# Kernel tuning notes

Hardware: AMD Instinct MI355X
Metric: run time of the kernel (lower is better)

Reference implementation:

```python
import jax, jax.numpy as jnp
import numpy as np

N, M, C, CSKIP, K = 16384, 4096, 256, 128, 3
BIG = 1e10  # distance penalty for cross-batch pairs


def setup_inputs() -> dict:
    key = jax.random.key(0)
    ks = jax.random.split(key, 6)
    return {
        "x": jax.random.normal(ks[0], (M, C), jnp.float32),
        "pos": jax.random.normal(ks[1], (M, 3), jnp.float32),
        "batch": jnp.zeros((M,), jnp.int32),
        "x_skip": jax.random.normal(ks[2], (N, CSKIP), jnp.float32),
        "pos_skip": jax.random.normal(ks[3], (N, 3), jnp.float32),
        "batch_skip": jnp.zeros((N,), jnp.int32),
        "W1": jax.random.normal(ks[4], (C + CSKIP, 256), jnp.float32) * (1.0 / np.sqrt(C + CSKIP)),
        "b1": jnp.zeros((256,), jnp.float32),
        "W2": jax.random.normal(ks[5], (256, 256), jnp.float32) * (1.0 / np.sqrt(256)),
        "b2": jnp.zeros((256,), jnp.float32),
    }


def _knn_idx(pos, pos_skip, batch, batch_skip, k):
    # Squared distances via GEMM form: [N, M]
    a2 = jnp.sum(pos_skip * pos_skip, axis=-1, keepdims=True)      # [N,1]
    b2 = jnp.sum(pos * pos, axis=-1)[None, :]                       # [1,M]
    d2 = a2 + b2 - 2.0 * (pos_skip @ pos.T)                         # [N,M]
    d2 = jnp.where(batch_skip[:, None] != batch[None, :], BIG, d2)
    _, idx = jax.lax.top_k(-d2, k)                                  # [N,k]
    return idx


def reference(x, pos, batch, x_skip, pos_skip, batch_skip, W1, b1, W2, b2):
    idx = _knn_idx(pos, pos_skip, batch, batch_skip, K)             # [N,k] coarse neighbor ids
    # Exact squared dist recomputed from gathered positions (matches torch diff path)
    diff = pos_skip[:, None, :] - pos[idx]                          # [N,k,3]
    d2 = jnp.sum(diff * diff, axis=-1, keepdims=True)               # [N,k,1]
    w = 1.0 / (d2 + 1e-8)                                           # inverse-distance weights
    wsum = jnp.sum(w, axis=1, keepdims=True)                        # per-row scatter_add == sum over k
    w = w / (wsum + 1e-8)
    x_interp = jnp.sum(w * x[idx], axis=1)                          # [N,C]
    h = jnp.concatenate([x_interp, x_skip], axis=1)                 # [N,C+C']
    h = jax.nn.relu(h @ W1 + b1)
    h = jax.nn.relu(h @ W2 + b2)
    return h
```

## Files before the change

### kernel.cpp

```cpp
#include <hip/hip_runtime.h>

typedef float     f4   __attribute__((ext_vector_type(4)));
typedef float     f32x4 __attribute__((ext_vector_type(4)));
typedef _Float16  h8   __attribute__((ext_vector_type(8)));
typedef _Float16  h4   __attribute__((ext_vector_type(4)));
typedef int       i4   __attribute__((ext_vector_type(4)));

#define NQ   16384
#define MP   4096
#define CF   256
#define CSK  128
#define K1   384
#define HID  256
#define QB   16

__global__ __launch_bounds__(256) void knn_kernel(
    const float* __restrict__ pos,
    const float* __restrict__ pos_skip,
    int*   __restrict__ idx_out,
    float* __restrict__ w_out)
{
    __shared__ float          px[MP];
    __shared__ float          py[MP];
    __shared__ float          pz[MP];
    __shared__ unsigned short ci[QB][96];
    __shared__ unsigned short ci2[QB][16][3];

    const int tid = threadIdx.x;

    for (int j = tid; j < MP; j += 256) {
        px[j] = pos[3*j+0];
        py[j] = pos[3*j+1];
        pz[j] = pos[3*j+2];
    }
    __syncthreads();

    const int lane = tid & 63;
    const int wv   = tid >> 6;

    float qx[4], qy[4], qz[4];
    #pragma unroll
    for (int k = 0; k < 4; k++) {
        const int q = blockIdx.x * QB + wv * 4 + k;
        qx[k] = pos_skip[3*q+0];
        qy[k] = pos_skip[3*q+1];
        qz[k] = pos_skip[3*q+2];
    }

    unsigned K0[4], K1v[4], K2[4];
    #pragma unroll
    for (int k = 0; k < 4; k++) { K0[k] = ~0u; K1v[k] = ~0u; K2[k] = ~0u; }

    #define EVAL(PX, PY, PZ, J)                                               \
        _Pragma("unroll")                                                     \
        for (int k = 0; k < 4; k++) {                                         \
            const float dx = qx[k] - (PX), dy = qy[k] - (PY),                 \
                        dz = qz[k] - (PZ);                                    \
            const float dd = fmaf(dx, dx, fmaf(dy, dy, dz * dz));             \
            const unsigned key = (__float_as_uint(dd) & 0xFFFFF000u) | (J);   \
            const unsigned h0 = max(K0[k], key);                              \
            K0[k] = min(K0[k], key);                                          \
            const unsigned n1 = min(K1v[k], h0);                              \
            const unsigned h1 = max(K1v[k], h0);                              \
            K1v[k] = n1;                                                      \
            K2[k] = min(K2[k], h1);                                           \
        }

    float c0x = px[lane],       c1x = px[lane + 64],
          c2x = px[lane + 128], c3x = px[lane + 192];
    float c0y = py[lane],       c1y = py[lane + 64],
          c2y = py[lane + 128], c3y = py[lane + 192];
    float c0z = pz[lane],       c1z = pz[lane + 64],
          c2z = pz[lane + 128], c3z = pz[lane + 192];

    for (int it = 0; it < 64; it += 4) {
        const unsigned jb = it * 64 + lane;
        const float nx0 = px[jb + 256], nx1 = px[jb + 320],
                    nx2 = px[jb + 384], nx3 = px[jb + 448];
        const float ny0 = py[jb + 256], ny1 = py[jb + 320],
                    ny2 = py[jb + 384], ny3 = py[jb + 448];
        const float nz0 = pz[jb + 256], nz1 = pz[jb + 320],
                    nz2 = pz[jb + 384], nz3 = pz[jb + 448];
        EVAL(c0x, c0y, c0z, jb);
        EVAL(c1x, c1y, c1z, jb + 64);
        EVAL(c2x, c2y, c2z, jb + 128);
        EVAL(c3x, c3y, c3z, jb + 192);
        c0x = nx0; c1x = nx1; c2x = nx2; c3x = nx3;
        c0y = ny0; c1y = ny1; c2y = ny2; c3y = ny3;
        c0z = nz0; c1z = nz1; c2z = nz2; c3z = nz3;
    }
    #undef EVAL

    #pragma unroll
    for (int k = 0; k < 4; k++) {
        const unsigned b0 = (unsigned)__builtin_amdgcn_ds_swizzle((int)K0[k],  0x041F);
        const unsigned b1 = (unsigned)__builtin_amdgcn_ds_swizzle((int)K1v[k], 0x041F);
        const unsigned b2 = (unsigned)__builtin_amdgcn_ds_swizzle((int)K2[k],  0x041F);
        const unsigned m0 = min(K0[k], b0);
        const unsigned c1 = max(K0[k], b0);
        const unsigned d0 = min(K1v[k], b1), d1 = max(K1v[k], b1);
        const unsigned m1 = min(c1, d0);
        const unsigned m2 = min(min(max(c1, d0), d1), min(K2[k], b2));
        if (!(lane & 1)) {
            const int q = wv * 4 + k;
            const int pr = lane >> 1;
            ci[q][pr*3+0] = (unsigned short)(m0 & 0xFFFu);
            ci[q][pr*3+1] = (unsigned short)(m1 & 0xFFFu);
            ci[q][pr*3+2] = (unsigned short)(m2 & 0xFFFu);
        }
    }
    __syncthreads();

    {
        const int q    = tid >> 4;
        const int part = tid & 15;
        const int g    = blockIdx.x * QB + q;
        const double qxd = (double)pos_skip[3*g+0];
        const double qyd = (double)pos_skip[3*g+1];
        const double qzd = (double)pos_skip[3*g+2];
        const double a2d = qxd*qxd + qyd*qyd + qzd*qzd;

        double e0 = 1e300, e1 = 1e300, e2 = 1e300;
        int    j0 = 0,     j1 = 0,     j2 = 0;
        #pragma unroll
        for (int c = 0; c < 6; c++) {
            const int j = ci[q][part*6 + c];
            const double pxd = (double)px[j], pyd = (double)py[j],
                         pzd = (double)pz[j];
            const double b2  = pxd*pxd + pyd*pyd + pzd*pzd;
            const double dot = qxd*pxd + qyd*pyd + qzd*pzd;
            const double d   = (a2d + b2) - 2.0 * dot;
            if (d < e2) {
                if (d < e1) {
                    e2 = e1; j2 = j1;
                    if (d < e0) { e1 = e0; j1 = j0; e0 = d; j0 = j; }
                    else        { e1 = d;  j1 = j; }
                } else { e2 = d; j2 = j; }
            }
        }
        ci2[q][part][0] = (unsigned short)j0;
        ci2[q][part][1] = (unsigned short)j1;
        ci2[q][part][2] = (unsigned short)j2;
    }
    __syncthreads();

    if (tid < QB) {
        const int g = blockIdx.x * QB + tid;
        const double qxd = (double)pos_skip[3*g+0];
        const double qyd = (double)pos_skip[3*g+1];
        const double qzd = (double)pos_skip[3*g+2];
        const double a2d = qxd*qxd + qyd*qyd + qzd*qzd;

        double e0 = 1e300, e1 = 1e300, e2 = 1e300;
        int    j0 = 0,     j1 = 0,     j2 = 0;
        for (int p = 0; p < 16; p++) {
            #pragma unroll
            for (int s = 0; s < 3; s++) {
                const int j = ci2[tid][p][s];
                const double pxd = (double)px[j], pyd = (double)py[j],
                             pzd = (double)pz[j];
                const double b2  = pxd*pxd + pyd*pyd + pzd*pzd;
                const double dot = qxd*pxd + qyd*pyd + qzd*pzd;
                const double d   = (a2d + b2) - 2.0 * dot;
                if (d < e2) {
                    if (d < e1) {
                        e2 = e1; j2 = j1;
                        if (d < e0) { e1 = e0; j1 = j0; e0 = d; j0 = j; }
                        else        { e1 = d;  j1 = j; }
                    } else { e2 = d; j2 = j; }
                }
            }
        }
        const float sx = pos_skip[3*g+0], sy = pos_skip[3*g+1], sz = pos_skip[3*g+2];
        const int jj[3] = { j0, j1, j2 };
        float wv3[3];
        #pragma unroll
        for (int k = 0; k < 3; k++) {
            const float dx = sx - px[jj[k]], dy = sy - py[jj[k]],
                        dz = sz - pz[jj[k]];
            const float dd = dx*dx + dy*dy + dz*dz;
            wv3[k] = 1.0f / (dd + 1e-8f);
        }
        const float inv = 1.0f / (wv3[0] + wv3[1] + wv3[2] + 1e-8f);
        #pragma unroll
        for (int k = 0; k < 3; k++) {
            idx_out[g*3+k] = jj[k];
            w_out[g*3+k]   = wv3[k] * inv;
        }
    }
}

__global__ __launch_bounds__(256) void wconv_kernel(
    const float* __restrict__ W1, const float* __restrict__ W2,
    _Float16* __restrict__ Wt1, _Float16* __restrict__ Wt2)
{
    const int i = blockIdx.x * 256 + threadIdx.x;
    if (i < K1 * HID) {
        const int k = i >> 8, n = i & 255;
        Wt1[(size_t)(k >> 5) * 8192 + ((k >> 3) & 3) * 2048 + n * 8 + (k & 7)]
            = (_Float16)W1[i];
    } else {
        const int i2 = i - K1 * HID;
        const int k = i2 >> 8, n = i2 & 255;
        Wt2[(size_t)(k >> 5) * 8192 + ((k >> 3) & 3) * 2048 + n * 8 + (k & 7)]
            = (_Float16)W2[i2];
    }
}

__global__ __launch_bounds__(256) void mlp_kernel(
    const float* __restrict__ x,
    const float* __restrict__ x_skip,
    const _Float16* __restrict__ Wt1,
    const _Float16* __restrict__ Wt2,
    const float* __restrict__ b1,
    const float* __restrict__ b2,
    const int*   __restrict__ nidx,
    const float* __restrict__ nw,
    float* __restrict__ out)
{
    __shared__ _Float16 As[32][392];
    _Float16 (*Hs)[264] = reinterpret_cast<_Float16 (*)[264]>(&As[0][0]);

    const int tid  = threadIdx.x;
    const int row0 = blockIdx.x * 32;

    {
        const int r   = tid >> 3;
        const int sub = tid & 7;
        const int g   = row0 + r;
        const int j0 = nidx[g*3+0], j1 = nidx[g*3+1], j2 = nidx[g*3+2];
        const float w0 = nw[g*3+0], w1 = nw[g*3+1], w2 = nw[g*3+2];
        const f4* xa = (const f4*)(x + (size_t)j0 * CF);
        const f4* xb = (const f4*)(x + (size_t)j1 * CF);
        const f4* xc = (const f4*)(x + (size_t)j2 * CF);
        const f4* xs = (const f4*)(x_skip + (size_t)g * CSK);
        #pragma unroll
        for (int t = 0; t < 8; t++) {
            const int c4 = t * 8 + sub;
            const f4 a = xa[c4], b = xb[c4], c = xc[c4];
            const f4 v = a * w0 + b * w1 + c * w2;
            h4 hv; hv[0]=(_Float16)v[0]; hv[1]=(_Float16)v[1];
                   hv[2]=(_Float16)v[2]; hv[3]=(_Float16)v[3];
            *(h4*)&As[r][c4 * 4] = hv;
        }
        #pragma unroll
        for (int t = 0; t < 4; t++) {
            const int c4 = t * 8 + sub;
            const f4 v = xs[c4];
            h4 hv; hv[0]=(_Float16)v[0]; hv[1]=(_Float16)v[1];
                   hv[2]=(_Float16)v[2]; hv[3]=(_Float16)v[3];
            *(h4*)&As[r][CF + c4 * 4] = hv;
        }
    }

    const int ln   = tid & 15;
    const int quad = (tid >> 4) & 3;
    const int wv_  = tid >> 6;
    const int nb   = wv_ * 64;
    const int q8   = quad * 8;

    const _Float16* w1b = Wt1 + quad * 2048 + (size_t)(nb + ln) * 8;
    const _Float16* w2b = Wt2 + quad * 2048 + (size_t)(nb + ln) * 8;

    f32x4 acc[2][4];
    #pragma unroll
    for (int mt = 0; mt < 2; mt++)
        #pragma unroll
        for (int nt = 0; nt < 4; nt++) acc[mt][nt] = (f32x4)0.0f;

    h8 B[3][4];
    #pragma unroll
    for (int s = 0; s < 3; s++)
        #pragma unroll
        for (int nt = 0; nt < 4; nt++)
            B[s][nt] = *(const h8*)(w1b + (size_t)s * 8192 + nt * 128);

    __syncthreads();

    #pragma unroll
    for (int kb = 0; kb < 12; kb++) {
        const int s = kb % 3;
        h8 ha[2];
        #pragma unroll
        for (int mt = 0; mt < 2; mt++)
            ha[mt] = *(const h8*)&As[mt*16 + ln][kb*32 + q8];
        h8 hb[4];
        #pragma unroll
        for (int nt = 0; nt < 4; nt++) hb[nt] = B[s][nt];
        if (kb < 9) {
            #pragma unroll
            for (int nt = 0; nt < 4; nt++)
                B[s][nt] = *(const h8*)(w1b + (size_t)(kb+3) * 8192 + nt * 128);
        } else {
            #pragma unroll
            for (int nt = 0; nt < 4; nt++)
                B[s][nt] = *(const h8*)(w2b + (size_t)(kb-9) * 8192 + nt * 128);
        }
        #pragma unroll
        for (int mt = 0; mt < 2; mt++)
            #pragma unroll
            for (int nt = 0; nt < 4; nt++)
                acc[mt][nt] = __builtin_amdgcn_mfma_f32_16x16x32_f16(
                    ha[mt], hb[nt], acc[mt][nt], 0, 0, 0);
    }
    __syncthreads();

    #pragma unroll
    for (int nt = 0; nt < 4; nt++) {
        const int n = nb + nt*16 + ln;
        const float bv = b1[n];
        #pragma unroll
        for (int mt = 0; mt < 2; mt++) {
            #pragma unroll
            for (int r = 0; r < 4; r++) {
                const int m = mt*16 + quad*4 + r;
                Hs[m][n] = (_Float16)fmaxf(acc[mt][nt][r] + bv, 0.0f);
            }
            acc[mt][nt] = (f32x4)0.0f;
        }
    }
    __syncthreads();

    #pragma unroll
    for (int kb = 0; kb < 8; kb++) {
        const int s = kb % 3;
        h8 ha[2];
        #pragma unroll
        for (int mt = 0; mt < 2; mt++)
            ha[mt] = *(const h8*)&Hs[mt*16 + ln][kb*32 + q8];
        h8 hb[4];
        #pragma unroll
        for (int nt = 0; nt < 4; nt++) hb[nt] = B[s][nt];
        if (kb < 5) {
            #pragma unroll
            for (int nt = 0; nt < 4; nt++)
                B[s][nt] = *(const h8*)(w2b + (size_t)(kb+3) * 8192 + nt * 128);
        }
        #pragma unroll
        for (int mt = 0; mt < 2; mt++)
            #pragma unroll
            for (int nt = 0; nt < 4; nt++)
                acc[mt][nt] = __builtin_amdgcn_mfma_f32_16x16x32_f16(
                    ha[mt], hb[nt], acc[mt][nt], 0, 0, 0);
    }

    #pragma unroll
    for (int nt = 0; nt < 4; nt++) {
        const int n = nb + nt*16 + ln;
        const float bv = b2[n];
        #pragma unroll
        for (int mt = 0; mt < 2; mt++)
            #pragma unroll
            for (int r = 0; r < 4; r++) {
                const int m = mt*16 + quad*4 + r;
                out[(size_t)(row0 + m) * HID + n] = fmaxf(acc[mt][nt][r] + bv, 0.0f);
            }
    }
}

extern "C" void kernel_launch(void* const* d_in, const int* in_sizes, int n_in,
                              void* d_out, int out_size, void* d_ws, size_t ws_size,
                              hipStream_t stream) {
    const float* x         = (const float*)d_in[0];
    const float* pos       = (const float*)d_in[1];
    const float* x_skip    = (const float*)d_in[3];
    const float* pos_skip  = (const float*)d_in[4];
    const float* W1        = (const float*)d_in[6];
    const float* b1        = (const float*)d_in[7];
    const float* W2        = (const float*)d_in[8];
    const float* b2        = (const float*)d_in[9];
    float* out = (float*)d_out;

    char* ws = (char*)d_ws;
    int*      nidx = (int*)ws;
    float*    nw   = (float*)(ws + 196608);
    _Float16* Wt1  = (_Float16*)(ws + 393216);
    _Float16* Wt2  = (_Float16*)(ws + 589824);

    wconv_kernel<<<(K1*HID + HID*HID) / 256, 256, 0, stream>>>(W1, W2, Wt1, Wt2);
    knn_kernel<<<NQ / QB, 256, 0, stream>>>(pos, pos_skip, nidx, nw);
    mlp_kernel<<<NQ / 32, 256, 0, stream>>>(x, x_skip, Wt1, Wt2, b1, b2, nidx, nw, out);
}
```

Baseline: 129.7 us.

## Fuse weight conversion into kNN, store positions as fp16, widen MLP blocks

The standalone weight-conversion launch is removed and its work spread across the first 1024 kNN blocks, 160 elements each. kNN candidate positions are now held in shared memory as fp16 (xy packed plus z), which halves LDS footprint and traffic, while the fp64 refinement stages read positions straight from global memory. The MLP kernel now processes 64 rows per block with 512 threads, so each weight fragment load is shared by more rows. The fp16 coarse distances may lose accuracy in candidate selection, and the refinement stages now pay global-memory gathers instead of LDS reads.

```diff
diff --git a/kernel.cpp b/kernel.cpp
--- a/kernel.cpp
+++ b/kernel.cpp
@@ -4,6 +4,7 @@
 typedef float     f32x4 __attribute__((ext_vector_type(4)));
 typedef _Float16  h8   __attribute__((ext_vector_type(8)));
 typedef _Float16  h4   __attribute__((ext_vector_type(4)));
+typedef _Float16  h2   __attribute__((ext_vector_type(2)));
 typedef int       i4   __attribute__((ext_vector_type(4)));
 
 #define NQ   16384
@@ -17,21 +18,40 @@
 __global__ __launch_bounds__(256) void knn_kernel(
     const float* __restrict__ pos,
     const float* __restrict__ pos_skip,
+    const float* __restrict__ W1,
+    const float* __restrict__ W2,
+    _Float16* __restrict__ Wt1,
+    _Float16* __restrict__ Wt2,
     int*   __restrict__ idx_out,
     float* __restrict__ w_out)
 {
-    __shared__ float          px[MP];
-    __shared__ float          py[MP];
-    __shared__ float          pz[MP];
+    __shared__ h2             hxy[MP];
+    __shared__ _Float16       hz[MP];
     __shared__ unsigned short ci[QB][96];
     __shared__ unsigned short ci2[QB][16][3];
 
     const int tid = threadIdx.x;
 
+    {
+        const int i = blockIdx.x * 160 + tid;
+        if (tid < 160) {
+            if (i < K1 * HID) {
+                const int k = i >> 8, n = i & 255;
+                Wt1[(size_t)(k >> 5) * 8192 + ((k >> 3) & 3) * 2048 + n * 8 + (k & 7)]
+                    = (_Float16)W1[i];
+            } else {
+                const int i2 = i - K1 * HID;
+                const int k = i2 >> 8, n = i2 & 255;
+                Wt2[(size_t)(k >> 5) * 8192 + ((k >> 3) & 3) * 2048 + n * 8 + (k & 7)]
+                    = (_Float16)W2[i2];
+            }
+        }
+    }
+
     for (int j = tid; j < MP; j += 256) {
-        px[j] = pos[3*j+0];
-        py[j] = pos[3*j+1];
-        pz[j] = pos[3*j+2];
+        h2 v; v[0] = (_Float16)pos[3*j+0]; v[1] = (_Float16)pos[3*j+1];
+        hxy[j] = v;
+        hz[j]  = (_Float16)pos[3*j+2];
     }
     __syncthreads();
 
@@ -51,45 +71,44 @@
     #pragma unroll
     for (int k = 0; k < 4; k++) { K0[k] = ~0u; K1v[k] = ~0u; K2[k] = ~0u; }
 
-    #define EVAL(PX, PY, PZ, J)                                               \
-        _Pragma("unroll")                                                     \
-        for (int k = 0; k < 4; k++) {                                         \
-            const float dx = qx[k] - (PX), dy = qy[k] - (PY),                 \
-                        dz = qz[k] - (PZ);                                    \
-            const float dd = fmaf(dx, dx, fmaf(dy, dy, dz * dz));             \
-            const unsigned key = (__float_as_uint(dd) & 0xFFFFF000u) | (J);   \
-            const unsigned h0 = max(K0[k], key);                              \
-            K0[k] = min(K0[k], key);                                          \
-            const unsigned n1 = min(K1v[k], h0);                              \
-            const unsigned h1 = max(K1v[k], h0);                              \
-            K1v[k] = n1;                                                      \
-            K2[k] = min(K2[k], h1);                                           \
-        }
-
-    float c0x = px[lane],       c1x = px[lane + 64],
-          c2x = px[lane + 128], c3x = px[lane + 192];
-    float c0y = py[lane],       c1y = py[lane + 64],
-          c2y = py[lane + 128], c3y = py[lane + 192];
-    float c0z = pz[lane],       c1z = pz[lane + 64],
-          c2z = pz[lane + 128], c3z = pz[lane + 192];
+    #define EVALP(XY, Z, J)                                                   \
+        {                                                                     \
+            const float fx = (float)(XY)[0], fy = (float)(XY)[1],             \
+                        fz = (float)(Z);                                      \
+            _Pragma("unroll")                                                 \
+            for (int k = 0; k < 4; k++) {                                     \
+                const float dx = qx[k] - fx, dy = qy[k] - fy,                 \
+                            dz = qz[k] - fz;                                  \
+                const float dd = fmaf(dx, dx, fmaf(dy, dy, dz * dz));         \
+                const unsigned key = (__float_as_uint(dd) & 0xFFFFF000u) | (J);\
+                const unsigned h0 = max(K0[k], key);                          \
+                K0[k] = min(K0[k], key);                                      \
+                const unsigned n1 = min(K1v[k], h0);                          \
+                const unsigned h1 = max(K1v[k], h0);                          \
+                K1v[k] = n1;                                                  \
+                K2[k] = min(K2[k], h1);                                       \
+            }                                                                 \
+        }
+
+    h2 cxy0 = hxy[lane],       cxy1 = hxy[lane + 64],
+       cxy2 = hxy[lane + 128], cxy3 = hxy[lane + 192];
+    _Float16 cz0 = hz[lane],       cz1 = hz[lane + 64],
+             cz2 = hz[lane + 128], cz3 = hz[lane + 192];
 
     for (int it = 0; it < 64; it += 4) {
         const unsigned jb = it * 64 + lane;
-        const float nx0 = px[jb + 256], nx1 = px[jb + 320],
-                    nx2 = px[jb + 384], nx3 = px[jb + 448];
-        const float ny0 = py[jb + 256], ny1 = py[jb + 320],
-                    ny2 = py[jb + 384], ny3 = py[jb + 448];
-        const float nz0 = pz[jb + 256], nz1 = pz[jb + 320],
-                    nz2 = pz[jb + 384], nz3 = pz[jb + 448];
-        EVAL(c0x, c0y, c0z, jb);
-        EVAL(c1x, c1y, c1z, jb + 64);
-        EVAL(c2x, c2y, c2z, jb + 128);
-        EVAL(c3x, c3y, c3z, jb + 192);
-        c0x = nx0; c1x = nx1; c2x = nx2; c3x = nx3;
-        c0y = ny0; c1y = ny1; c2y = ny2; c3y = ny3;
-        c0z = nz0; c1z = nz1; c2z = nz2; c3z = nz3;
-    }
-    #undef EVAL
+        const h2 nxy0 = hxy[jb + 256], nxy1 = hxy[jb + 320],
+                 nxy2 = hxy[jb + 384], nxy3 = hxy[jb + 448];
+        const _Float16 nz0 = hz[jb + 256], nz1 = hz[jb + 320],
+                       nz2 = hz[jb + 384], nz3 = hz[jb + 448];
+        EVALP(cxy0, cz0, jb);
+        EVALP(cxy1, cz1, jb + 64);
+        EVALP(cxy2, cz2, jb + 128);
+        EVALP(cxy3, cz3, jb + 192);
+        cxy0 = nxy0; cxy1 = nxy1; cxy2 = nxy2; cxy3 = nxy3;
+        cz0 = nz0; cz1 = nz1; cz2 = nz2; cz3 = nz3;
+    }
+    #undef EVALP
 
     #pragma unroll
     for (int k = 0; k < 4; k++) {
@@ -125,8 +144,8 @@
         #pragma unroll
         for (int c = 0; c < 6; c++) {
             const int j = ci[q][part*6 + c];
-            const double pxd = (double)px[j], pyd = (double)py[j],
-                         pzd = (double)pz[j];
+            const double pxd = (double)pos[3*j+0], pyd = (double)pos[3*j+1],
+                         pzd = (double)pos[3*j+2];
             const double b2  = pxd*pxd + pyd*pyd + pzd*pzd;
             const double dot = qxd*pxd + qyd*pyd + qzd*pzd;
             const double d   = (a2d + b2) - 2.0 * dot;
@@ -157,8 +176,8 @@
             #pragma unroll
             for (int s = 0; s < 3; s++) {
                 const int j = ci2[tid][p][s];
-                const double pxd = (double)px[j], pyd = (double)py[j],
-                             pzd = (double)pz[j];
+                const double pxd = (double)pos[3*j+0], pyd = (double)pos[3*j+1],
+                             pzd = (double)pos[3*j+2];
                 const double b2  = pxd*pxd + pyd*pyd + pzd*pzd;
                 const double dot = qxd*pxd + qyd*pyd + qzd*pzd;
                 const double d   = (a2d + b2) - 2.0 * dot;
@@ -176,8 +195,8 @@
         float wv3[3];
         #pragma unroll
         for (int k = 0; k < 3; k++) {
-            const float dx = sx - px[jj[k]], dy = sy - py[jj[k]],
-                        dz = sz - pz[jj[k]];
+            const float dx = sx - pos[3*jj[k]+0], dy = sy - pos[3*jj[k]+1],
+                        dz = sz - pos[3*jj[k]+2];
             const float dd = dx*dx + dy*dy + dz*dz;
             wv3[k] = 1.0f / (dd + 1e-8f);
         }
@@ -190,24 +209,7 @@
     }
 }
 
-__global__ __launch_bounds__(256) void wconv_kernel(
-    const float* __restrict__ W1, const float* __restrict__ W2,
-    _Float16* __restrict__ Wt1, _Float16* __restrict__ Wt2)
-{
-    const int i = blockIdx.x * 256 + threadIdx.x;
-    if (i < K1 * HID) {
-        const int k = i >> 8, n = i & 255;
-        Wt1[(size_t)(k >> 5) * 8192 + ((k >> 3) & 3) * 2048 + n * 8 + (k & 7)]
-            = (_Float16)W1[i];
-    } else {
-        const int i2 = i - K1 * HID;
-        const int k = i2 >> 8, n = i2 & 255;
-        Wt2[(size_t)(k >> 5) * 8192 + ((k >> 3) & 3) * 2048 + n * 8 + (k & 7)]
-            = (_Float16)W2[i2];
-    }
-}
-
-__global__ __launch_bounds__(256) void mlp_kernel(
+__global__ __launch_bounds__(512) void mlp_kernel(
     const float* __restrict__ x,
     const float* __restrict__ x_skip,
     const _Float16* __restrict__ Wt1,
@@ -218,11 +220,11 @@
     const float* __restrict__ nw,
     float* __restrict__ out)
 {
-    __shared__ _Float16 As[32][392];
+    __shared__ _Float16 As[64][392];
     _Float16 (*Hs)[264] = reinterpret_cast<_Float16 (*)[264]>(&As[0][0]);
 
     const int tid  = threadIdx.x;
-    const int row0 = blockIdx.x * 32;
+    const int row0 = blockIdx.x * 64;
 
     {
         const int r   = tid >> 3;
@@ -256,7 +258,8 @@
     const int ln   = tid & 15;
     const int quad = (tid >> 4) & 3;
     const int wv_  = tid >> 6;
-    const int nb   = wv_ * 64;
+    const int nb   = (wv_ & 3) * 64;
+    const int mb   = (wv_ >> 2) * 32;
     const int q8   = quad * 8;
 
     const _Float16* w1b = Wt1 + quad * 2048 + (size_t)(nb + ln) * 8;
@@ -283,7 +286,7 @@
         h8 ha[2];
         #pragma unroll
         for (int mt = 0; mt < 2; mt++)
-            ha[mt] = *(const h8*)&As[mt*16 + ln][kb*32 + q8];
+            ha[mt] = *(const h8*)&As[mb + mt*16 + ln][kb*32 + q8];
         h8 hb[4];
         #pragma unroll
         for (int nt = 0; nt < 4; nt++) hb[nt] = B[s][nt];
@@ -313,7 +316,7 @@
         for (int mt = 0; mt < 2; mt++) {
             #pragma unroll
             for (int r = 0; r < 4; r++) {
-                const int m = mt*16 + quad*4 + r;
+                const int m = mb + mt*16 + quad*4 + r;
                 Hs[m][n] = (_Float16)fmaxf(acc[mt][nt][r] + bv, 0.0f);
             }
             acc[mt][nt] = (f32x4)0.0f;
@@ -327,7 +330,7 @@
         h8 ha[2];
         #pragma unroll
         for (int mt = 0; mt < 2; mt++)
-            ha[mt] = *(const h8*)&Hs[mt*16 + ln][kb*32 + q8];
+            ha[mt] = *(const h8*)&Hs[mb + mt*16 + ln][kb*32 + q8];
         h8 hb[4];
         #pragma unroll
         for (int nt = 0; nt < 4; nt++) hb[nt] = B[s][nt];
@@ -352,7 +355,7 @@
         for (int mt = 0; mt < 2; mt++)
             #pragma unroll
             for (int r = 0; r < 4; r++) {
-                const int m = mt*16 + quad*4 + r;
+                const int m = mb + mt*16 + quad*4 + r;
                 out[(size_t)(row0 + m) * HID + n] = fmaxf(acc[mt][nt][r] + bv, 0.0f);
             }
     }
@@ -377,7 +380,8 @@
     _Float16* Wt1  = (_Float16*)(ws + 393216);
     _Float16* Wt2  = (_Float16*)(ws + 589824);
 
-    wconv_kernel<<<(K1*HID + HID*HID) / 256, 256, 0, stream>>>(W1, W2, Wt1, Wt2);
-    knn_kernel<<<NQ / QB, 256, 0, stream>>>(pos, pos_skip, nidx, nw);
-    mlp_kernel<<<NQ / 32, 256, 0, stream>>>(x, x_skip, Wt1, Wt2, b1, b2, nidx, nw, out);
+    knn_kernel<<<NQ / QB, 256, 0, stream>>>(pos, pos_skip, W1, W2, Wt1, Wt2,
+                                            nidx, nw);
+    mlp_kernel<<<NQ / 64, 512, 0, stream>>>(x, x_skip, Wt1, Wt2, b1, b2,
+                                            nidx, nw, out);
 }
```

Measured after the change: 136.2 us. +5.0%, slower.
